# Performance work log

Measured on AMD Instinct MI355X. Metric: run time of the kernel, lower is better.

The kernel has to match this reference:

```python
import jax, jax.numpy as jnp
import numpy as np

HEADS = 4
HEAD_DIM = 24
PH, PW = 2, 2  # proposal grid -> M = PH*PW = 4 prototype centers
EPS = 1e-12


def setup_inputs() -> dict:
    key = jax.random.key(0)
    ks = jax.random.split(key, 6)
    B, Cin, H, W = 16, 128, 112, 112
    Cout = 128
    D = HEADS * HEAD_DIM  # 96
    x = jax.random.normal(ks[0], (B, Cin, H, W), jnp.float32)
    # 1x1 conv weights stored as [out, in] (kernel dims squeezed)
    f_w = jax.random.normal(ks[1], (D, Cin), jnp.float32) / np.float32(np.sqrt(Cin))
    f_b = jnp.zeros((D,), jnp.float32)
    v_w = jax.random.normal(ks[2], (D, Cin), jnp.float32) / np.float32(np.sqrt(Cin))
    v_b = jnp.zeros((D,), jnp.float32)
    proj_w = jax.random.normal(ks[3], (Cout, D), jnp.float32) / np.float32(np.sqrt(D))
    proj_b = jnp.zeros((Cout,), jnp.float32)
    sim_alpha = jnp.ones((1,), jnp.float32)
    sim_beta = jnp.zeros((1,), jnp.float32)
    # OrthogonalPriorGenerator: Gram-Schmidt orthonormalized random rows
    rng = np.random.default_rng(0)
    W0 = rng.standard_normal((HEAD_DIM, PH * PW)).astype(np.float32) * np.sqrt(2.0 / HEAD_DIM).astype(np.float32)
    q, _ = np.linalg.qr(W0)  # orthonormal columns
    centers = jnp.asarray(q.T, jnp.float32)  # [M, head_dim], orthonormal rows
    return {"x": x, "f_w": f_w, "f_b": f_b, "v_w": v_w, "v_b": v_b,
            "proj_w": proj_w, "proj_b": proj_b,
            "sim_alpha": sim_alpha, "sim_beta": sim_beta, "centers": centers}


def reference(x, f_w, f_b, v_w, v_b, proj_w, proj_b, sim_alpha, sim_beta, centers):
    B, Cin, H, W = x.shape
    M = PH * PW
    c = HEAD_DIM
    bh = B * HEADS
    n = H * W
    # 1x1 convs
    f = jnp.einsum('oi,bihw->bohw', f_w, x) + f_b[None, :, None, None]
    v = jnp.einsum('oi,bihw->bohw', v_w, x) + v_b[None, :, None, None]
    # split heads into batch: b (e c) h w -> (b e) c h w
    f = f.reshape(bh, c, n)                      # [(be), c, n]
    v4 = v.reshape(bh, c, H, W)                  # [(be), c, h, w]
    # adaptive avg pool to (PH, PW) -> value centers [(be), M, c]
    vc = v4.reshape(bh, c, PH, H // PH, PW, W // PW).mean(axis=(3, 5))
    value_centers = vc.reshape(bh, c, M).transpose(0, 2, 1)
    # cosine similarity of orthonormal centers vs tokens
    cn = centers / jnp.maximum(jnp.linalg.norm(centers, axis=-1, keepdims=True), EPS)
    xn = f.transpose(0, 2, 1)                    # [(be), n, c]
    xn = xn / jnp.maximum(jnp.linalg.norm(xn, axis=-1, keepdims=True), EPS)
    sim = jax.nn.sigmoid(sim_beta + sim_alpha * jnp.einsum('mc,bnc->bmn', cn, xn))
    # hard top-1 assignment mask over centers
    idx = jnp.argmax(sim, axis=1)                # [(be), n]
    mask = jax.nn.one_hot(idx, M, axis=1, dtype=sim.dtype)  # [(be), M, n]
    sim = sim * mask
    # dispatch: weighted aggregation into centers
    value2 = v4.reshape(bh, c, n).transpose(0, 2, 1)          # [(be), n, c]
    agg = (jnp.einsum('bmn,bnc->bmc', sim, value2) + value_centers)
    agg = agg / (sim.sum(axis=-1, keepdims=True) + 1.0)
    # combine: redistribute center features back to tokens
    out = jnp.einsum('bmn,bmc->bnc', sim, agg)                # [(be), n, c]
    out = out.transpose(0, 2, 1).reshape(B, HEADS * c, H, W)  # merge heads
    out = jnp.einsum('oi,bihw->bohw', proj_w, out) + proj_b[None, :, None, None]
    assignment_map = idx[0].reshape(H, W)
    return out, assignment_map
```

## Files before the change

kernel.cpp:

```cpp
#include <hip/hip_runtime.h>
#include <hip/hip_bf16.h>

namespace {

constexpr int kCin   = 128;
constexpr int kHW    = 12544;
constexpr int kW     = 112;
constexpr int kGrps  = 49;
constexpr size_t kOut1Off = (size_t)16 * 128 * kHW;

__device__ __forceinline__ float bf2f(unsigned short u) {
  union { unsigned int i; float f; } v;
  v.i = ((unsigned int)u) << 16;
  return v.f;
}

__device__ __forceinline__ unsigned short f2bf(float f) {
  union { float f; unsigned int i; } v;
  v.f = f;
  unsigned int x = v.i;
  x += 0x7fffu + ((x >> 16) & 1u);
  return (unsigned short)(x >> 16);
}

template <bool BF>
__device__ __forceinline__ float ld1(const void* p, size_t i) {
  if constexpr (BF) return bf2f(((const unsigned short*)p)[i]);
  else              return ((const float*)p)[i];
}
template <bool BF>
__device__ __forceinline__ void ld4(const void* p, size_t i, float o[4]) {
  if constexpr (BF) {
    const ushort4 u = *reinterpret_cast<const ushort4*>((const unsigned short*)p + i);
    o[0] = bf2f(u.x); o[1] = bf2f(u.y); o[2] = bf2f(u.z); o[3] = bf2f(u.w);
  } else {
    const float4 u = *reinterpret_cast<const float4*>((const float*)p + i);
    o[0] = u.x; o[1] = u.y; o[2] = u.z; o[3] = u.w;
  }
}
template <bool BF>
__device__ __forceinline__ void st1(void* p, size_t i, float v) {
  if constexpr (BF) ((unsigned short*)p)[i] = f2bf(v);
  else              ((float*)p)[i] = v;
}

__global__ void detect_dtype(const unsigned short* __restrict__ fw, int* __restrict__ flag) {
  __shared__ int cnt_s;
  if (threadIdx.x == 0) cnt_s = 0;
  __syncthreads();
  int c = 0;
  for (int i = threadIdx.x; i < 4096; i += 256) {
    const float v = bf2f(fw[i]);
    if (fabsf(v) > 4.0f) ++c;
  }
  atomicAdd(&cnt_s, c);
  __syncthreads();
  if (threadIdx.x == 0) flag[0] = (cnt_s > 100) ? 0 : 1;
}

struct SMain {
  float fh[96 * 65];
  float cn[4][24];
  float s[4][64];
  unsigned char idx[4][64];
  unsigned char q[64];
};

template <bool BF>
__device__ __forceinline__ void main_body(
    SMain& sm,
    const void* __restrict__ x,  const void* __restrict__ f_w, const void* __restrict__ f_b,
    const void* __restrict__ v_w, const void* __restrict__ v_b,
    const void* __restrict__ sim_alpha, const void* __restrict__ sim_beta,
    const void* __restrict__ centers,
    void* __restrict__ out0,
    float* __restrict__ aggsum, float* __restrict__ vpool, float* __restrict__ cnt)
{
  const int tid = threadIdx.x;
  const int b   = blockIdx.x / kGrps;
  const int grp = blockIdx.x % kGrps;

  if (tid < 4) {
    float cv[24];
    float n2 = 0.f;
#pragma unroll
    for (int c = 0; c < 24; ++c) { cv[c] = ld1<BF>(centers, tid * 24 + c); n2 += cv[c] * cv[c]; }
    const float inv = 1.f / fmaxf(sqrtf(n2), 1e-12f);
#pragma unroll
    for (int c = 0; c < 24; ++c) sm.cn[tid][c] = cv[c] * inv;
  }
  const float alpha = ld1<BF>(sim_alpha, 0);
  const float beta  = ld1<BF>(sim_beta, 0);

  const int ty = tid >> 4;
  const int tx = tid & 15;
  const bool is_f = (ty < 8);
  const void*  wsel  = is_f ? f_w : v_w;
  const void*  bsel  = is_f ? f_b : v_b;
  const size_t wrow0 = (size_t)(is_f ? ty * 12 : ty * 12 - 96);
  float bias[12];
#pragma unroll
  for (int r = 0; r < 12; ++r) bias[r] = ld1<BF>(bsel, wrow0 + r);

  const int e   = tid >> 6;
  const int tok = tid & 63;

  float agg_m[4]  = {0.f, 0.f, 0.f, 0.f};
  float pool_q[4] = {0.f, 0.f, 0.f, 0.f};
  float cacc = 0.f;

  __syncthreads();

  for (int t = 0; t < 4; ++t) {
    const int hw0 = (grp * 4 + t) * 64;

    float acc[12][4];
#pragma unroll
    for (int r = 0; r < 12; ++r)
#pragma unroll
      for (int j = 0; j < 4; ++j) acc[r][j] = 0.f;

    const size_t xbase = ((size_t)b * kCin) * kHW + hw0 + tx * 4;
    for (int i = 0; i < 128; i += 4) {
      float xv[4][4];
#pragma unroll
      for (int ci = 0; ci < 4; ++ci) ld4<BF>(x, xbase + (size_t)(i + ci) * kHW, xv[ci]);
      float wv[6][4];
#pragma unroll
      for (int r = 0; r < 6; ++r) ld4<BF>(wsel, (wrow0 + r) * 128 + i, wv[r]);
#pragma unroll
      for (int r = 0; r < 6; ++r)
#pragma unroll
        for (int ci = 0; ci < 4; ++ci)
#pragma unroll
          for (int j = 0; j < 4; ++j)
            acc[r][j] = fmaf(wv[r][ci], xv[ci][j], acc[r][j]);
#pragma unroll
      for (int r = 0; r < 6; ++r) ld4<BF>(wsel, (wrow0 + 6 + r) * 128 + i, wv[r]);
#pragma unroll
      for (int r = 0; r < 6; ++r)
#pragma unroll
        for (int ci = 0; ci < 4; ++ci)
#pragma unroll
          for (int j = 0; j < 4; ++j)
            acc[6 + r][j] = fmaf(wv[r][ci], xv[ci][j], acc[6 + r][j]);
    }

    if (is_f) {
#pragma unroll
      for (int r = 0; r < 12; ++r)
#pragma unroll
        for (int j = 0; j < 4; ++j)
          sm.fh[(ty * 12 + r) * 65 + tx * 4 + j] = acc[r][j] + bias[r];
    }
    __syncthreads();

    {
      float dm[4] = {0.f, 0.f, 0.f, 0.f};
      float n2 = 0.f;
#pragma unroll
      for (int c = 0; c < 24; ++c) {
        const float fc = sm.fh[(e * 24 + c) * 65 + tok];
        n2 += fc * fc;
        dm[0] += fc * sm.cn[0][c];
        dm[1] += fc * sm.cn[1][c];
        dm[2] += fc * sm.cn[2][c];
        dm[3] += fc * sm.cn[3][c];
      }
      const float inv = 1.f / fmaxf(sqrtf(n2), 1e-12f);
      float s[4];
#pragma unroll
      for (int m = 0; m < 4; ++m) {
        const float z = beta + alpha * dm[m] * inv;
        s[m] = 1.f / (1.f + __expf(-z));
      }
      float best = -1.f;
      int bi = 0;
#pragma unroll
      for (int m = 0; m < 4; ++m)
        if (s[m] > best) { best = s[m]; bi = m; }

      const int hw = hw0 + tok;
      st1<BF>(out0, ((size_t)(b * 128 + e)) * kHW + hw, best);
      st1<BF>(out0, ((size_t)(b * 128 + 4 + e)) * kHW + hw, (float)bi);
      sm.s[e][tok]   = best;
      sm.idx[e][tok] = (unsigned char)bi;
      if (e == 0) {
        const int h = hw / kW;
        const int w = hw - h * kW;
        sm.q[tok] = (unsigned char)((h >= 56 ? 2 : 0) + (w >= 56 ? 1 : 0));
      }
    }
    __syncthreads();

    if (!is_f) {
#pragma unroll
      for (int r = 0; r < 12; ++r)
#pragma unroll
        for (int j = 0; j < 4; ++j)
          sm.fh[((ty - 8) * 12 + r) * 65 + tx * 4 + j] = acc[r][j] + bias[r];
    }
    __syncthreads();

    if (tid < 192) {
      const int half = tid / 96;
      const int c    = tid - half * 96;
      const int eh   = c / 24;
      const int row0 = c * 65;
      const int t20  = half * 32;
      for (int k = 0; k < 32; ++k) {
        const int t2 = t20 + k;
        const float v = sm.fh[row0 + t2];
        const float s = sm.s[eh][t2];
        const int  mi = sm.idx[eh][t2];
        const int  q  = sm.q[t2];
        const float sv = s * v;
        agg_m[0]  += (mi == 0) ? sv : 0.f;
        agg_m[1]  += (mi == 1) ? sv : 0.f;
        agg_m[2]  += (mi == 2) ? sv : 0.f;
        agg_m[3]  += (mi == 3) ? sv : 0.f;
        pool_q[0] += (q == 0) ? v : 0.f;
        pool_q[1] += (q == 1) ? v : 0.f;
        pool_q[2] += (q == 2) ? v : 0.f;
        pool_q[3] += (q == 3) ? v : 0.f;
      }
    } else if (tid < 224) {
      const int p  = tid - 192;
      const int em = p >> 1;
      const int ce = em >> 2, cm = em & 3;
      const int t20 = (p & 1) * 32;
      for (int k = 0; k < 32; ++k) {
        const int t2 = t20 + k;
        cacc += (sm.idx[ce][t2] == cm) ? sm.s[ce][t2] : 0.f;
      }
    }
    __syncthreads();
  }

  if (tid < 192) {
    const int half = tid / 96;
    const int c  = tid - half * 96;
    const int eh = c / 24;
    const int cc = c % 24;
    const int bh = b * 4 + eh;
#pragma unroll
    for (int m = 0; m < 4; ++m) {
      atomicAdd(&aggsum[(bh * 4 + m) * 24 + cc], agg_m[m]);
      atomicAdd(&vpool[(bh * 4 + m) * 24 + cc], pool_q[m]);
    }
  } else if (tid < 224) {
    const int p  = tid - 192;
    const int em = p >> 1;
    atomicAdd(&cnt[b * 16 + em], cacc);
  }
}

__global__ __launch_bounds__(256, 4) void cluster_main(
    const int* __restrict__ flag,
    const void* x, const void* f_w, const void* f_b, const void* v_w, const void* v_b,
    const void* sim_alpha, const void* sim_beta, const void* centers,
    void* out0, float* aggsum, float* vpool, float* cnt)
{
  __shared__ SMain sm;
  if (*flag)
    main_body<true>(sm, x, f_w, f_b, v_w, v_b, sim_alpha, sim_beta, centers, out0, aggsum, vpool, cnt);
  else
    main_body<false>(sm, x, f_w, f_b, v_w, v_b, sim_alpha, sim_beta, centers, out0, aggsum, vpool, cnt);
}

template <bool BF>
__device__ __forceinline__ void ptab_body(
    float* __restrict__ af, const void* __restrict__ proj_w,
    const float* __restrict__ aggsum, const float* __restrict__ vpool,
    const float* __restrict__ cnt, float* __restrict__ ptab)
{
  const int b   = blockIdx.x;
  const int tid = threadIdx.x;
  for (int k = tid; k < 384; k += 256) {
    const int em = k / 24;
    af[k] = (aggsum[b * 384 + k] + vpool[b * 384 + k] * (1.f / 3136.f)) / (cnt[b * 16 + em] + 1.f);
  }
  __syncthreads();
#pragma unroll
  for (int i = 0; i < 8; ++i) {
    const int g  = i * 256 + tid;
    const int o  = g >> 4;
    const int em = g & 15;
    const int e  = em >> 2;
    float acc = 0.f;
#pragma unroll
    for (int c = 0; c < 24; ++c)
      acc = fmaf(ld1<BF>(proj_w, (size_t)o * 96 + e * 24 + c), af[em * 24 + c], acc);
    ptab[b * 2048 + g] = acc;
  }
}

__global__ void cluster_ptab(const int* __restrict__ flag, const void* proj_w,
                             const float* __restrict__ aggsum, const float* __restrict__ vpool,
                             const float* __restrict__ cnt, float* __restrict__ ptab) {
  __shared__ float af[384];
  if (*flag) ptab_body<true>(af, proj_w, aggsum, vpool, cnt, ptab);
  else       ptab_body<false>(af, proj_w, aggsum, vpool, cnt, ptab);
}

__global__ void cluster_amap(const int* __restrict__ flag, void* __restrict__ dout) {
  const int i = blockIdx.x * 256 + threadIdx.x;
  if (i >= kHW) return;
  const size_t src = (size_t)4 * kHW + i;
  if (*flag) {
    unsigned short* o = (unsigned short*)dout;
    o[kOut1Off + i] = o[src];
  } else {
    float* o = (float*)dout;
    o[kOut1Off + i] = o[src];
  }
}

struct SOut {
  float p[2048];
  float pb[128];
};

template <bool BF>
__device__ __forceinline__ void out_body(
    SOut& so, const float* __restrict__ ptab,
    const void* __restrict__ proj_b, void* __restrict__ out0)
{
  const int tid = threadIdx.x;
  const int b   = blockIdx.x / kGrps;
  const int grp = blockIdx.x % kGrps;
  const int hw  = grp * 256 + tid;

  for (int k = tid; k < 2048; k += 256) so.p[k] = ptab[b * 2048 + k];
  if (tid < 128) so.pb[tid] = ld1<BF>(proj_b, tid);
  __syncthreads();

  const size_t base = ((size_t)(b * 128)) * kHW + hw;
  float sv[4];
  int   mi[4];
#pragma unroll
  for (int e = 0; e < 4; ++e) {
    sv[e] = ld1<BF>(out0, base + (size_t)e * kHW);
    const float iv = ld1<BF>(out0, base + (size_t)(4 + e) * kHW);
    mi[e] = (int)(iv + 0.5f);
  }

#pragma unroll 4
  for (int o = 0; o < 128; ++o) {
    float a = so.pb[o];
    a = fmaf(sv[0], so.p[o * 16 +  0 + mi[0]], a);
    a = fmaf(sv[1], so.p[o * 16 +  4 + mi[1]], a);
    a = fmaf(sv[2], so.p[o * 16 +  8 + mi[2]], a);
    a = fmaf(sv[3], so.p[o * 16 + 12 + mi[3]], a);
    st1<BF>(out0, base + (size_t)o * kHW, a);
  }
}

__global__ __launch_bounds__(256) void cluster_out(
    const int* __restrict__ flag,
    const void* proj_b, const float* __restrict__ ptab, void* out0)
{
  __shared__ SOut so;
  if (*flag) out_body<true>(so, ptab, proj_b, out0);
  else       out_body<false>(so, ptab, proj_b, out0);
}

}

extern "C" void kernel_launch(void* const* d_in, const int* in_sizes, int n_in,
                              void* d_out, int out_size, void* d_ws, size_t ws_size,
                              hipStream_t stream) {
  const void* x         = d_in[0];
  const void* f_w       = d_in[1];
  const void* f_b       = d_in[2];
  const void* v_w       = d_in[3];
  const void* v_b       = d_in[4];
  const void* proj_w    = d_in[5];
  const void* proj_b    = d_in[6];
  const void* sim_alpha = d_in[7];
  const void* sim_beta  = d_in[8];
  const void* centers   = d_in[9];

  int*   flag   = (int*)d_ws;
  float* fws    = (float*)((char*)d_ws + 16);
  float* aggsum = fws;
  float* vpool  = fws + 6144;
  float* cnt    = fws + 12288;
  float* ptab   = fws + 12544;

  hipMemsetAsync(d_ws, 0, 16 + 12544 * sizeof(float), stream);

  detect_dtype<<<dim3(1), dim3(256), 0, stream>>>((const unsigned short*)f_w, flag);
  cluster_main<<<dim3(16 * kGrps), dim3(256), 0, stream>>>(
      flag, x, f_w, f_b, v_w, v_b, sim_alpha, sim_beta, centers,
      d_out, aggsum, vpool, cnt);
  cluster_ptab<<<dim3(16), dim3(256), 0, stream>>>(flag, proj_w, aggsum, vpool, cnt, ptab);
  cluster_amap<<<dim3(kGrps), dim3(256), 0, stream>>>(flag, d_out);
  cluster_out<<<dim3(16 * kGrps), dim3(256), 0, stream>>>(flag, proj_b, ptab, d_out);
}
```

Baseline: 513.0 us.

## Split main kernel into one 64-token tile per block and fold amap copy

The main kernel now launches one block per 64-token tile (196 tiles per batch) instead of looping over four tiles per block, which quadruples the grid and removes the per-tile loop and its extra barriers. The launch-bounds occupancy hint is raised from 4 to 6 blocks per unit. The separate assignment-map copy kernel is removed and its copy is folded into the output kernel for batch 0. In exchange, four times as many atomic adds go to the reduction buffers, and the higher occupancy hint may force register spilling of the 48-float accumulator.

Result: slower. 821.8 us (+60.2%).

```diff
diff --git a/kernel.cpp b/kernel.cpp
--- a/kernel.cpp
+++ b/kernel.cpp
@@ -7,6 +7,7 @@
 constexpr int kHW    = 12544;
 constexpr int kW     = 112;
 constexpr int kGrps  = 49;
+constexpr int kTiles = 196;
 constexpr size_t kOut1Off = (size_t)16 * 128 * kHW;
 
 __device__ __forceinline__ float bf2f(unsigned short u) {
@@ -76,9 +77,10 @@
     void* __restrict__ out0,
     float* __restrict__ aggsum, float* __restrict__ vpool, float* __restrict__ cnt)
 {
-  const int tid = threadIdx.x;
-  const int b   = blockIdx.x / kGrps;
-  const int grp = blockIdx.x % kGrps;
+  const int tid  = threadIdx.x;
+  const int b    = blockIdx.x / kTiles;
+  const int tile = blockIdx.x % kTiles;
+  const int hw0  = tile * 64;
 
   if (tid < 4) {
     float cv[24];
@@ -105,144 +107,124 @@
   const int e   = tid >> 6;
   const int tok = tid & 63;
 
+  __syncthreads();
+
+  float acc[12][4];
+#pragma unroll
+  for (int r = 0; r < 12; ++r)
+#pragma unroll
+    for (int j = 0; j < 4; ++j) acc[r][j] = 0.f;
+
+  const size_t xbase = ((size_t)b * kCin) * kHW + hw0 + tx * 4;
+  for (int i = 0; i < 128; i += 4) {
+    float xv[4][4];
+#pragma unroll
+    for (int ci = 0; ci < 4; ++ci) ld4<BF>(x, xbase + (size_t)(i + ci) * kHW, xv[ci]);
+    float wv[6][4];
+#pragma unroll
+    for (int r = 0; r < 6; ++r) ld4<BF>(wsel, (wrow0 + r) * 128 + i, wv[r]);
+#pragma unroll
+    for (int r = 0; r < 6; ++r)
+#pragma unroll
+      for (int ci = 0; ci < 4; ++ci)
+#pragma unroll
+        for (int j = 0; j < 4; ++j)
+          acc[r][j] = fmaf(wv[r][ci], xv[ci][j], acc[r][j]);
+#pragma unroll
+    for (int r = 0; r < 6; ++r) ld4<BF>(wsel, (wrow0 + 6 + r) * 128 + i, wv[r]);
+#pragma unroll
+    for (int r = 0; r < 6; ++r)
+#pragma unroll
+      for (int ci = 0; ci < 4; ++ci)
+#pragma unroll
+        for (int j = 0; j < 4; ++j)
+          acc[6 + r][j] = fmaf(wv[r][ci], xv[ci][j], acc[6 + r][j]);
+  }
+
+  if (is_f) {
+#pragma unroll
+    for (int r = 0; r < 12; ++r)
+#pragma unroll
+      for (int j = 0; j < 4; ++j)
+        sm.fh[(ty * 12 + r) * 65 + tx * 4 + j] = acc[r][j] + bias[r];
+  }
+  __syncthreads();
+
+  {
+    float dm[4] = {0.f, 0.f, 0.f, 0.f};
+    float n2 = 0.f;
+#pragma unroll
+    for (int c = 0; c < 24; ++c) {
+      const float fc = sm.fh[(e * 24 + c) * 65 + tok];
+      n2 += fc * fc;
+      dm[0] += fc * sm.cn[0][c];
+      dm[1] += fc * sm.cn[1][c];
+      dm[2] += fc * sm.cn[2][c];
+      dm[3] += fc * sm.cn[3][c];
+    }
+    const float inv = 1.f / fmaxf(sqrtf(n2), 1e-12f);
+    float s[4];
+#pragma unroll
+    for (int m = 0; m < 4; ++m) {
+      const float z = beta + alpha * dm[m] * inv;
+      s[m] = 1.f / (1.f + __expf(-z));
+    }
+    float best = -1.f;
+    int bi = 0;
+#pragma unroll
+    for (int m = 0; m < 4; ++m)
+      if (s[m] > best) { best = s[m]; bi = m; }
+
+    const int hw = hw0 + tok;
+    st1<BF>(out0, ((size_t)(b * 128 + e)) * kHW + hw, best);
+    st1<BF>(out0, ((size_t)(b * 128 + 4 + e)) * kHW + hw, (float)bi);
+    sm.s[e][tok]   = best;
+    sm.idx[e][tok] = (unsigned char)bi;
+    if (e == 0) {
+      const int h = hw / kW;
+      const int w = hw - h * kW;
+      sm.q[tok] = (unsigned char)((h >= 56 ? 2 : 0) + (w >= 56 ? 1 : 0));
+    }
+  }
+  __syncthreads();
+
+  if (!is_f) {
+#pragma unroll
+    for (int r = 0; r < 12; ++r)
+#pragma unroll
+      for (int j = 0; j < 4; ++j)
+        sm.fh[((ty - 8) * 12 + r) * 65 + tx * 4 + j] = acc[r][j] + bias[r];
+  }
+  __syncthreads();
+
   float agg_m[4]  = {0.f, 0.f, 0.f, 0.f};
   float pool_q[4] = {0.f, 0.f, 0.f, 0.f};
   float cacc = 0.f;
-
-  __syncthreads();
-
-  for (int t = 0; t < 4; ++t) {
-    const int hw0 = (grp * 4 + t) * 64;
-
-    float acc[12][4];
-#pragma unroll
-    for (int r = 0; r < 12; ++r)
-#pragma unroll
-      for (int j = 0; j < 4; ++j) acc[r][j] = 0.f;
-
-    const size_t xbase = ((size_t)b * kCin) * kHW + hw0 + tx * 4;
-    for (int i = 0; i < 128; i += 4) {
-      float xv[4][4];
-#pragma unroll
-      for (int ci = 0; ci < 4; ++ci) ld4<BF>(x, xbase + (size_t)(i + ci) * kHW, xv[ci]);
-      float wv[6][4];
-#pragma unroll
-      for (int r = 0; r < 6; ++r) ld4<BF>(wsel, (wrow0 + r) * 128 + i, wv[r]);
-#pragma unroll
-      for (int r = 0; r < 6; ++r)
-#pragma unroll
-        for (int ci = 0; ci < 4; ++ci)
-#pragma unroll
-          for (int j = 0; j < 4; ++j)
-            acc[r][j] = fmaf(wv[r][ci], xv[ci][j], acc[r][j]);
-#pragma unroll
-      for (int r = 0; r < 6; ++r) ld4<BF>(wsel, (wrow0 + 6 + r) * 128 + i, wv[r]);
-#pragma unroll
-      for (int r = 0; r < 6; ++r)
-#pragma unroll
-        for (int ci = 0; ci < 4; ++ci)
-#pragma unroll
-          for (int j = 0; j < 4; ++j)
-            acc[6 + r][j] = fmaf(wv[r][ci], xv[ci][j], acc[6 + r][j]);
-    }
-
-    if (is_f) {
-#pragma unroll
-      for (int r = 0; r < 12; ++r)
-#pragma unroll
-        for (int j = 0; j < 4; ++j)
-          sm.fh[(ty * 12 + r) * 65 + tx * 4 + j] = acc[r][j] + bias[r];
-    }
-    __syncthreads();
-
-    {
-      float dm[4] = {0.f, 0.f, 0.f, 0.f};
-      float n2 = 0.f;
-#pragma unroll
-      for (int c = 0; c < 24; ++c) {
-        const float fc = sm.fh[(e * 24 + c) * 65 + tok];
-        n2 += fc * fc;
-        dm[0] += fc * sm.cn[0][c];
-        dm[1] += fc * sm.cn[1][c];
-        dm[2] += fc * sm.cn[2][c];
-        dm[3] += fc * sm.cn[3][c];
-      }
-      const float inv = 1.f / fmaxf(sqrtf(n2), 1e-12f);
-      float s[4];
-#pragma unroll
-      for (int m = 0; m < 4; ++m) {
-        const float z = beta + alpha * dm[m] * inv;
-        s[m] = 1.f / (1.f + __expf(-z));
-      }
-      float best = -1.f;
-      int bi = 0;
-#pragma unroll
-      for (int m = 0; m < 4; ++m)
-        if (s[m] > best) { best = s[m]; bi = m; }
-
-      const int hw = hw0 + tok;
-      st1<BF>(out0, ((size_t)(b * 128 + e)) * kHW + hw, best);
-      st1<BF>(out0, ((size_t)(b * 128 + 4 + e)) * kHW + hw, (float)bi);
-      sm.s[e][tok]   = best;
-      sm.idx[e][tok] = (unsigned char)bi;
-      if (e == 0) {
-        const int h = hw / kW;
-        const int w = hw - h * kW;
-        sm.q[tok] = (unsigned char)((h >= 56 ? 2 : 0) + (w >= 56 ? 1 : 0));
-      }
-    }
-    __syncthreads();
-
-    if (!is_f) {
-#pragma unroll
-      for (int r = 0; r < 12; ++r)
-#pragma unroll
-        for (int j = 0; j < 4; ++j)
-          sm.fh[((ty - 8) * 12 + r) * 65 + tx * 4 + j] = acc[r][j] + bias[r];
-    }
-    __syncthreads();
-
-    if (tid < 192) {
-      const int half = tid / 96;
-      const int c    = tid - half * 96;
-      const int eh   = c / 24;
-      const int row0 = c * 65;
-      const int t20  = half * 32;
-      for (int k = 0; k < 32; ++k) {
-        const int t2 = t20 + k;
-        const float v = sm.fh[row0 + t2];
-        const float s = sm.s[eh][t2];
-        const int  mi = sm.idx[eh][t2];
-        const int  q  = sm.q[t2];
-        const float sv = s * v;
-        agg_m[0]  += (mi == 0) ? sv : 0.f;
-        agg_m[1]  += (mi == 1) ? sv : 0.f;
-        agg_m[2]  += (mi == 2) ? sv : 0.f;
-        agg_m[3]  += (mi == 3) ? sv : 0.f;
-        pool_q[0] += (q == 0) ? v : 0.f;
-        pool_q[1] += (q == 1) ? v : 0.f;
-        pool_q[2] += (q == 2) ? v : 0.f;
-        pool_q[3] += (q == 3) ? v : 0.f;
-      }
-    } else if (tid < 224) {
-      const int p  = tid - 192;
-      const int em = p >> 1;
-      const int ce = em >> 2, cm = em & 3;
-      const int t20 = (p & 1) * 32;
-      for (int k = 0; k < 32; ++k) {
-        const int t2 = t20 + k;
-        cacc += (sm.idx[ce][t2] == cm) ? sm.s[ce][t2] : 0.f;
-      }
-    }
-    __syncthreads();
-  }
-
   if (tid < 192) {
     const int half = tid / 96;
-    const int c  = tid - half * 96;
-    const int eh = c / 24;
-    const int cc = c % 24;
-    const int bh = b * 4 + eh;
+    const int c    = tid - half * 96;
+    const int eh   = c / 24;
+    const int row0 = c * 65;
+    const int t20  = half * 32;
+    for (int k = 0; k < 32; ++k) {
+      const int t2 = t20 + k;
+      const float v = sm.fh[row0 + t2];
+      const float s = sm.s[eh][t2];
+      const int  mi = sm.idx[eh][t2];
+      const int  q  = sm.q[t2];
+      const float sv = s * v;
+      agg_m[0]  += (mi == 0) ? sv : 0.f;
+      agg_m[1]  += (mi == 1) ? sv : 0.f;
+      agg_m[2]  += (mi == 2) ? sv : 0.f;
+      agg_m[3]  += (mi == 3) ? sv : 0.f;
+      pool_q[0] += (q == 0) ? v : 0.f;
+      pool_q[1] += (q == 1) ? v : 0.f;
+      pool_q[2] += (q == 2) ? v : 0.f;
+      pool_q[3] += (q == 3) ? v : 0.f;
+    }
+    const int eh2 = c / 24;
+    const int cc  = c % 24;
+    const int bh  = b * 4 + eh2;
 #pragma unroll
     for (int m = 0; m < 4; ++m) {
       atomicAdd(&aggsum[(bh * 4 + m) * 24 + cc], agg_m[m]);
@@ -251,11 +233,17 @@
   } else if (tid < 224) {
     const int p  = tid - 192;
     const int em = p >> 1;
+    const int ce = em >> 2, cm = em & 3;
+    const int t20 = (p & 1) * 32;
+    for (int k = 0; k < 32; ++k) {
+      const int t2 = t20 + k;
+      cacc += (sm.idx[ce][t2] == cm) ? sm.s[ce][t2] : 0.f;
+    }
     atomicAdd(&cnt[b * 16 + em], cacc);
   }
 }
 
-__global__ __launch_bounds__(256, 4) void cluster_main(
+__global__ __launch_bounds__(256, 6) void cluster_main(
     const int* __restrict__ flag,
     const void* x, const void* f_w, const void* f_b, const void* v_w, const void* v_b,
     const void* sim_alpha, const void* sim_beta, const void* centers,
@@ -303,19 +291,6 @@
   else       ptab_body<false>(af, proj_w, aggsum, vpool, cnt, ptab);
 }
 
-__global__ void cluster_amap(const int* __restrict__ flag, void* __restrict__ dout) {
-  const int i = blockIdx.x * 256 + threadIdx.x;
-  if (i >= kHW) return;
-  const size_t src = (size_t)4 * kHW + i;
-  if (*flag) {
-    unsigned short* o = (unsigned short*)dout;
-    o[kOut1Off + i] = o[src];
-  } else {
-    float* o = (float*)dout;
-    o[kOut1Off + i] = o[src];
-  }
-}
-
 struct SOut {
   float p[2048];
   float pb[128];
@@ -338,11 +313,16 @@
   const size_t base = ((size_t)(b * 128)) * kHW + hw;
   float sv[4];
   int   mi[4];
+  float iv0 = 0.f;
 #pragma unroll
   for (int e = 0; e < 4; ++e) {
     sv[e] = ld1<BF>(out0, base + (size_t)e * kHW);
     const float iv = ld1<BF>(out0, base + (size_t)(4 + e) * kHW);
+    if (e == 0) iv0 = iv;
     mi[e] = (int)(iv + 0.5f);
+  }
+  if (b == 0) {
+    st1<BF>(out0, kOut1Off + hw, iv0);
   }
 
 #pragma unroll 4
@@ -391,10 +371,9 @@
   hipMemsetAsync(d_ws, 0, 16 + 12544 * sizeof(float), stream);
 
   detect_dtype<<<dim3(1), dim3(256), 0, stream>>>((const unsigned short*)f_w, flag);
-  cluster_main<<<dim3(16 * kGrps), dim3(256), 0, stream>>>(
+  cluster_main<<<dim3(16 * kTiles), dim3(256), 0, stream>>>(
       flag, x, f_w, f_b, v_w, v_b, sim_alpha, sim_beta, centers,
       d_out, aggsum, vpool, cnt);
   cluster_ptab<<<dim3(16), dim3(256), 0, stream>>>(flag, proj_w, aggsum, vpool, cnt, ptab);
-  cluster_amap<<<dim3(kGrps), dim3(256), 0, stream>>>(flag, d_out);
   cluster_out<<<dim3(16 * kGrps), dim3(256), 0, stream>>>(flag, proj_b, ptab, d_out);
 }
```
